# Performance work log

Measured on AMD Instinct MI355X. Metric: run time of the kernel, lower is better.

The kernel has to match this reference:

```python
import jax, jax.numpy as jnp
import numpy as np

N, D_IN, D_OUT = 4096, 1024, 1024

def setup_inputs() -> dict:
    key = jax.random.key(0)
    ks = jax.random.split(key, 7)
    s = 1.0 / np.sqrt(D_IN)
    return {
        "x": jax.random.normal(ks[0], (N, D_IN), dtype=jnp.float32),
        "W1": jax.random.normal(ks[1], (D_OUT, D_IN), dtype=jnp.float32) * s,
        "b1": jax.random.normal(ks[2], (D_OUT,), dtype=jnp.float32) * 0.01,
        "W2": jax.random.normal(ks[3], (D_OUT, D_IN), dtype=jnp.float32) * s,
        "b2": jax.random.normal(ks[4], (D_OUT,), dtype=jnp.float32) * 0.01,
        "W3": jax.random.normal(ks[5], (D_OUT, D_IN), dtype=jnp.float32) * s,
        "b3": jax.random.normal(ks[6], (D_OUT,), dtype=jnp.float32) * 0.01,
        "output_dim": D_OUT,
    }

def reference(x, W1, b1, W2, b2, W3, b3, output_dim):
    # q, k, v: [N, D_OUT]  (torch Linear: x @ W.T + b)
    q = x @ W1.T + b1
    k = x @ W2.T + b2
    v = x @ W3.T + b3
    # NOTE: original computes K @ Q^T (not Q @ K^T) — keep faithful.
    scale = 1.0 / jnp.sqrt(jnp.asarray(output_dim, dtype=x.dtype))
    attn = jax.nn.softmax(jnp.einsum("nd,md->nm", k, q) * scale, axis=-1)  # [N, N]
    # value.unsqueeze(0) * attn.unsqueeze(-1) summed over axis 1 == attn @ v
    return attn @ v  # [N, D_OUT]
```

## Files before the change

kernel.cpp:

```cpp
#include <hip/hip_runtime.h>


typedef short bf16x8 __attribute__((ext_vector_type(8)));
typedef float f32x4  __attribute__((ext_vector_type(4)));

struct FalseT { static constexpr bool value = false; };
struct TrueT  { static constexpr bool value = true;  };

__device__ __forceinline__ short f2bf(float f) {
    unsigned u = __builtin_bit_cast(unsigned, f);
    u += 0x7FFFu + ((u >> 16) & 1u);
    return (short)(u >> 16);
}
__device__ __forceinline__ float bf2f(short s) {
    return __builtin_bit_cast(float, (unsigned)((unsigned short)s) << 16);
}

__device__ __forceinline__ void gld_lds16(const short* g, short* l) {
    __builtin_amdgcn_global_load_lds(
        (const __attribute__((address_space(1))) void*)g,
        (__attribute__((address_space(3))) void*)l, 16, 0, 0);
}

#define WAITV(n) asm volatile("s_waitcnt vmcnt(" #n ")" ::: "memory")
#define LGKM0()  do { asm volatile("s_waitcnt lgkmcnt(0)" ::: "memory"); \
                      __builtin_amdgcn_sched_barrier(0); } while (0)
#define LGKM8()  asm volatile("s_waitcnt lgkmcnt(8)" ::: "memory")
#define BAR()    __builtin_amdgcn_s_barrier()

template<int CMODE>
__global__ __launch_bounds__(512)
void gemm256(const short* __restrict__ A, int lda,
             const short* __restrict__ B, int ldb,
             const float* __restrict__ bias,
             short* __restrict__ Cout, int ldc, float scale,
             int K, size_t zstride)
{
    __shared__ __align__(16) short As[2][2][128 * 64];
    __shared__ __align__(16) short Bs[2][2][128 * 64];

    const int tid  = threadIdx.x;
    const int lane = tid & 63;
    const int wave = tid >> 6;
    const int wr   = wave >> 2;
    const int wc   = wave & 3;
    const int quad = lane >> 4;
    const int l16  = lane & 15;
    const size_t bm0 = (size_t)blockIdx.y * 256;
    const size_t bn0 = (size_t)blockIdx.x * 256;
    const int koff = blockIdx.z * K;

    f32x4 acc[8][4] = {};

    const int srow  = lane >> 3;
    const int sgran = (lane & 7) ^ srow;
    const short* Ag0 = A + (bm0 + wave * 16 + srow) * (size_t)lda + koff + sgran * 8;
    const short* Ag1 = Ag0 + (size_t)128 * lda;
    const short* Bg0 = B + (bn0 + wave * 16 + srow) * (size_t)ldb + koff + sgran * 8;
    const short* Bg1 = Bg0 + (size_t)128 * ldb;

    const int s0   = ((quad ^ (l16 & 7)) << 3);
    const int s1   = (((4 + quad) ^ (l16 & 7)) << 3);
    const int rdA0 = (wr * 64 + l16) * 64;
    const int rdB0 = (wc * 32 + l16) * 64;

    auto stage = [&](short* half, const short* g, int ld, int kt) {
#pragma unroll
        for (int i = 0; i < 2; ++i)
            gld_lds16(g + (size_t)(i * 8) * ld + kt,
                      half + (wave * 16 + i * 8) * 64);
    };

    bf16x8 af[4][2], bfr0[2][2], bfr1[2][2];

    auto ldAf = [&](const short* Ah) {
#pragma unroll
        for (int m4 = 0; m4 < 4; ++m4) {
            af[m4][0] = *(const bf16x8*)(Ah + rdA0 + m4 * 1024 + s0);
            af[m4][1] = *(const bf16x8*)(Ah + rdA0 + m4 * 1024 + s1);
        }
    };
    auto ldBf = [&](bf16x8 (&bx)[2][2], const short* Bh) {
#pragma unroll
        for (int n2 = 0; n2 < 2; ++n2) {
            bx[n2][0] = *(const bf16x8*)(Bh + rdB0 + n2 * 1024 + s0);
            bx[n2][1] = *(const bf16x8*)(Bh + rdB0 + n2 * 1024 + s1);
        }
    };
    auto mm = [&](int mq, int nq, bf16x8 (&bx)[2][2]) {
        __builtin_amdgcn_s_setprio(1);
#pragma unroll
        for (int ks = 0; ks < 2; ++ks)
#pragma unroll
            for (int m4 = 0; m4 < 4; ++m4)
#pragma unroll
                for (int n2 = 0; n2 < 2; ++n2)
                    acc[mq * 4 + m4][nq * 2 + n2] =
                        __builtin_amdgcn_mfma_f32_16x16x32_bf16(
                            af[m4][ks], bx[n2][ks],
                            acc[mq * 4 + m4][nq * 2 + n2], 0, 0, 0);
        __builtin_amdgcn_s_setprio(0);
    };

    stage(&As[0][0][0], Ag0, lda, 0);
    stage(&Bs[0][0][0], Bg0, ldb, 0);
    stage(&Bs[0][1][0], Bg1, ldb, 0);
    stage(&As[0][1][0], Ag1, lda, 0);
    stage(&As[1][0][0], Ag0, lda, 64);
    stage(&Bs[1][0][0], Bg0, ldb, 64);
    stage(&Bs[1][1][0], Bg1, ldb, 64);
    WAITV(6);
    BAR();
    __builtin_amdgcn_sched_barrier(0);

    int kt = 0;
    auto iterbody = [&](auto LASTC) {
        constexpr bool LAST = decltype(LASTC)::value;
        ldAf(&As[0][0][0]);
        ldBf(bfr0, &Bs[0][0][0]);
        stage(&As[1][1][0], Ag1, lda, kt + 64);
        LGKM8();
        BAR();
        LGKM0();
        mm(0, 0, bfr0);
        BAR();
        ldBf(bfr1, &Bs[0][1][0]);
        if constexpr (!LAST) stage(&As[0][0][0], Ag0, lda, kt + 128);
        BAR();
        LGKM0();
        mm(0, 1, bfr1);
        BAR();
        ldAf(&As[0][1][0]);
        if constexpr (!LAST) stage(&Bs[0][0][0], Bg0, ldb, kt + 128);
        BAR();
        LGKM0();
        mm(1, 1, bfr1);
        BAR();
        if constexpr (!LAST) stage(&Bs[0][1][0], Bg1, ldb, kt + 128);
        mm(1, 0, bfr0);
        if constexpr (LAST) { WAITV(0); } else { WAITV(6); }
        BAR();
        ldAf(&As[1][0][0]);
        ldBf(bfr0, &Bs[1][0][0]);
        if constexpr (!LAST) stage(&As[0][1][0], Ag1, lda, kt + 128);
        LGKM8();
        BAR();
        LGKM0();
        mm(0, 0, bfr0);
        BAR();
        ldBf(bfr1, &Bs[1][1][0]);
        if constexpr (!LAST) stage(&As[1][0][0], Ag0, lda, kt + 192);
        BAR();
        LGKM0();
        mm(0, 1, bfr1);
        BAR();
        ldAf(&As[1][1][0]);
        if constexpr (!LAST) stage(&Bs[1][0][0], Bg0, ldb, kt + 192);
        BAR();
        LGKM0();
        mm(1, 1, bfr1);
        BAR();
        if constexpr (!LAST) stage(&Bs[1][1][0], Bg1, ldb, kt + 192);
        mm(1, 0, bfr0);
        if constexpr (!LAST) { WAITV(6); }
        BAR();
    };

    const int nfull = (K >> 7) - 1;
    for (int i = 0; i < nfull; ++i) {
        iterbody(FalseT{});
        kt += 128;
    }
    iterbody(TrueT{});

    short* Cs = Cout + ((CMODE == 3) ? (size_t)blockIdx.z * zstride : 0);
#pragma unroll
    for (int mt = 0; mt < 8; ++mt) {
        const int mq = mt >> 2, m4 = mt & 3;
#pragma unroll
        for (int nt = 0; nt < 4; ++nt) {
            const int nq = nt >> 1, n2 = nt & 1;
            const size_t col = bn0 + nq * 128 + wc * 32 + n2 * 16 + l16;
            const float bc = (CMODE == 0) ? bias[col] : 0.0f;
#pragma unroll
            for (int r = 0; r < 4; ++r) {
                const size_t row = bm0 + mq * 128 + wr * 64 + m4 * 16 + quad * 4 + r;
                float v = acc[mt][nt][r] * scale + bc;
                if (CMODE == 2) v = __expf(v);
                Cs[row * (size_t)ldc + col] = f2bf(v);
            }
        }
    }
}

__global__ __launch_bounds__(256)
void transpose_v(const short* __restrict__ qkv, short* __restrict__ vt)
{
    __shared__ short sh[64][72];
    const int n0 = blockIdx.x * 64, d0 = blockIdx.y * 64;
    const int t = threadIdx.x;
    const int r = t >> 2, c = (t & 3) << 4;

    const short* src = qkv + (size_t)(n0 + r) * 3072 + 2048 + d0 + c;
    *(int4*)(&sh[r][c])     = *(const int4*)(src);
    *(int4*)(&sh[r][c + 8]) = *(const int4*)(src + 8);
    __syncthreads();

    short tmp[16];
#pragma unroll
    for (int j = 0; j < 16; j++) tmp[j] = sh[c + j][r];
    short* dst = vt + (size_t)(d0 + r) * 4096 + n0 + c;
    *(int4*)(dst)     = *(const int4*)(tmp);
    *(int4*)(dst + 8) = *(const int4*)(tmp + 8);
}

__global__ __launch_bounds__(256)
void reduce4div(const short* __restrict__ E, const short* __restrict__ outp,
                float* __restrict__ out)
{
    const int row = blockIdx.x;
    const int t = threadIdx.x;
    const int wave = t >> 6, lane = t & 63;

    const short* e = E + (size_t)row * 4096 + (t << 4);
    short sh[16];
    *(int4*)(sh)     = *(const int4*)(e);
    *(int4*)(sh + 8) = *(const int4*)(e + 8);
    float s = 0.0f;
#pragma unroll
    for (int i = 0; i < 16; i++) s += bf2f(sh[i]);
#pragma unroll
    for (int off = 32; off; off >>= 1) s += __shfl_down(s, off);
    __shared__ float red[4];
    if (lane == 0) red[wave] = s;
    __syncthreads();
    const float inv = 1.0f / (red[0] + red[1] + red[2] + red[3]);

    const size_t base = (size_t)row * 1024 + (t << 2);
    float a[4] = {0.0f, 0.0f, 0.0f, 0.0f};
#pragma unroll
    for (int z = 0; z < 4; z++) {
        short4 p = *(const short4*)(outp + z * (size_t)4096 * 1024 + base);
        a[0] += bf2f(p.x); a[1] += bf2f(p.y);
        a[2] += bf2f(p.z); a[3] += bf2f(p.w);
    }
    float4 o;
    o.x = a[0] * inv; o.y = a[1] * inv; o.z = a[2] * inv; o.w = a[3] * inv;
    *(float4*)(out + base) = o;
}

__global__ __launch_bounds__(256)
void prep(const float* __restrict__ x, const float* __restrict__ W1,
          const float* __restrict__ W2, const float* __restrict__ W3,
          const float* __restrict__ b1, const float* __restrict__ b2,
          const float* __restrict__ b3,
          short* __restrict__ xb, short* __restrict__ Wb,
          float* __restrict__ bcat)
{
    const int i = blockIdx.x * 256 + threadIdx.x;
    const int NX = 1048576;
    const int NW = 262144;
    if (i < NX + 3 * NW) {
        const float* src; short* dst; int j;
        if (i < NX)               { src = x;  dst = xb; j = i; }
        else if (i < NX + NW)     { src = W1; dst = Wb; j = i - NX; }
        else if (i < NX + 2 * NW) { src = W2; dst = Wb + 1048576; j = i - NX - NW; }
        else                      { src = W3; dst = Wb + 2097152; j = i - NX - 2 * NW; }
        const float4 f = ((const float4*)src)[j];
        short4 o;
        o.x = f2bf(f.x); o.y = f2bf(f.y); o.z = f2bf(f.z); o.w = f2bf(f.w);
        *(short4*)(dst + (j << 2)) = o;
    } else {
        const int j = i - (NX + 3 * NW);
        if (j < 3072)
            bcat[j] = (j < 1024) ? b1[j] : (j < 2048 ? b2[j - 1024] : b3[j - 2048]);
    }
}

extern "C" void kernel_launch(void* const* d_in, const int* in_sizes, int n_in,
                              void* d_out, int out_size, void* d_ws, size_t ws_size,
                              hipStream_t stream)
{
    const float* x  = (const float*)d_in[0];
    const float* W1 = (const float*)d_in[1];
    const float* b1 = (const float*)d_in[2];
    const float* W2 = (const float*)d_in[3];
    const float* b2 = (const float*)d_in[4];
    const float* W3 = (const float*)d_in[5];
    const float* b3 = (const float*)d_in[6];
    float* out = (float*)d_out;

    const int N = 4096, D = 1024;

    char* wsb = (char*)d_ws;
    short* vt   = (short*)wsb;
    short* E    = (short*)(wsb + (size_t)8  * 1024 * 1024);
    short* xb   = (short*)(wsb + (size_t)40 * 1024 * 1024);
    short* Wb   = (short*)(wsb + (size_t)48 * 1024 * 1024);
    float* bcat = (float*)(wsb + (size_t)54 * 1024 * 1024);
    short* qkv  = (short*)(wsb + (size_t)54 * 1024 * 1024 + 16384);
    short* outp = (short*)(wsb + (size_t)40 * 1024 * 1024);

    prep<<<(1048576 + 3 * 262144 + 3072 + 255) / 256, 256, 0, stream>>>(
        x, W1, W2, W3, b1, b2, b3, xb, Wb, bcat);

    dim3 gqkv(3 * D / 256, N / 256);
    gemm256<0><<<gqkv, 512, 0, stream>>>(xb, D, Wb, D, bcat,
                                         qkv, 3 * D, 1.0f, D, 0);

    dim3 gt(N / 64, D / 64);
    transpose_v<<<gt, 256, 0, stream>>>(qkv, vt);

    dim3 gs(N / 256, N / 256);
    gemm256<2><<<gs, 512, 0, stream>>>(qkv + D, 3 * D, qkv, 3 * D,
                                       nullptr, E, N, 0.03125f, D, 0);

    dim3 go(D / 256, N / 256, 4);
    gemm256<3><<<go, 512, 0, stream>>>(E, N, vt, N, nullptr,
                                       outp, D, 1.0f, N / 4,
                                       (size_t)N * D);

    reduce4div<<<N, 256, 0, stream>>>(E, outp, out);
}
```

Before: 218.0 us.

## Switch GEMM to 32x32x16 MFMA tiles and drop explicit LDS waits

Replaces the 16x16x32 bf16 MFMA tiling with 32x32x16 instructions, so each wave computes 2x1 32x32 fragments per quadrant with 16-wide accumulators. LDS fragment loads are restructured to match the new operand layout, and the epilogue row/column mapping is rewritten. The explicit lgkmcnt waits and several barriers around fragment loads are removed, leaving the compiler to insert LDS waits, with sched_barriers added after the vmcnt waits. The larger MFMA should cut instruction issue and LDS traffic per FLOP, but it changes the LDS bank-access pattern and risks less overlap or races from the fewer barriers.

```diff
diff --git a/kernel.cpp b/kernel.cpp
--- a/kernel.cpp
+++ b/kernel.cpp
@@ -2,7 +2,7 @@
 
 
 typedef short bf16x8 __attribute__((ext_vector_type(8)));
-typedef float f32x4  __attribute__((ext_vector_type(4)));
+typedef float f32x16 __attribute__((ext_vector_type(16)));
 
 struct FalseT { static constexpr bool value = false; };
 struct TrueT  { static constexpr bool value = true;  };
@@ -23,9 +23,6 @@
 }
 
 #define WAITV(n) asm volatile("s_waitcnt vmcnt(" #n ")" ::: "memory")
-#define LGKM0()  do { asm volatile("s_waitcnt lgkmcnt(0)" ::: "memory"); \
-                      __builtin_amdgcn_sched_barrier(0); } while (0)
-#define LGKM8()  asm volatile("s_waitcnt lgkmcnt(8)" ::: "memory")
 #define BAR()    __builtin_amdgcn_s_barrier()
 
 template<int CMODE>
@@ -44,13 +41,13 @@
     const int wave = tid >> 6;
     const int wr   = wave >> 2;
     const int wc   = wave & 3;
-    const int quad = lane >> 4;
-    const int l16  = lane & 15;
+    const int l32  = lane & 31;
+    const int khalf = lane >> 5;
     const size_t bm0 = (size_t)blockIdx.y * 256;
     const size_t bn0 = (size_t)blockIdx.x * 256;
     const int koff = blockIdx.z * K;
 
-    f32x4 acc[8][4] = {};
+    f32x16 acc[4][2] = {};
 
     const int srow  = lane >> 3;
     const int sgran = (lane & 7) ^ srow;
@@ -59,10 +56,9 @@
     const short* Bg0 = B + (bn0 + wave * 16 + srow) * (size_t)ldb + koff + sgran * 8;
     const short* Bg1 = Bg0 + (size_t)128 * ldb;
 
-    const int s0   = ((quad ^ (l16 & 7)) << 3);
-    const int s1   = (((4 + quad) ^ (l16 & 7)) << 3);
-    const int rdA0 = (wr * 64 + l16) * 64;
-    const int rdB0 = (wc * 32 + l16) * 64;
+    const int sx   = l32 & 7;
+    const int rdA0 = (wr * 64 + l32) * 64;
+    const int rdB0 = (wc * 32 + l32) * 64;
 
     auto stage = [&](short* half, const short* g, int ld, int kt) {
 #pragma unroll
@@ -71,34 +67,30 @@
                       half + (wave * 16 + i * 8) * 64);
     };
 
-    bf16x8 af[4][2], bfr0[2][2], bfr1[2][2];
-
-    auto ldAf = [&](const short* Ah) {
-#pragma unroll
-        for (int m4 = 0; m4 < 4; ++m4) {
-            af[m4][0] = *(const bf16x8*)(Ah + rdA0 + m4 * 1024 + s0);
-            af[m4][1] = *(const bf16x8*)(Ah + rdA0 + m4 * 1024 + s1);
-        }
-    };
-    auto ldBf = [&](bf16x8 (&bx)[2][2], const short* Bh) {
-#pragma unroll
-        for (int n2 = 0; n2 < 2; ++n2) {
-            bx[n2][0] = *(const bf16x8*)(Bh + rdB0 + n2 * 1024 + s0);
-            bx[n2][1] = *(const bf16x8*)(Bh + rdB0 + n2 * 1024 + s1);
-        }
-    };
-    auto mm = [&](int mq, int nq, bf16x8 (&bx)[2][2]) {
+    bf16x8 af[2][4], bfr0[4], bfr1[4];
+
+    auto ldA = [&](const short* Ah) {
+#pragma unroll
+        for (int f = 0; f < 2; ++f)
+#pragma unroll
+            for (int ks = 0; ks < 4; ++ks)
+                af[f][ks] = *(const bf16x8*)(
+                    Ah + rdA0 + f * 2048 + (((ks * 2 + khalf) ^ sx) << 3));
+    };
+    auto ldB = [&](bf16x8 (&bx)[4], const short* Bh) {
+#pragma unroll
+        for (int ks = 0; ks < 4; ++ks)
+            bx[ks] = *(const bf16x8*)(
+                Bh + rdB0 + (((ks * 2 + khalf) ^ sx) << 3));
+    };
+    auto mm = [&](int mq, int nq, bf16x8 (&bx)[4]) {
         __builtin_amdgcn_s_setprio(1);
 #pragma unroll
-        for (int ks = 0; ks < 2; ++ks)
-#pragma unroll
-            for (int m4 = 0; m4 < 4; ++m4)
-#pragma unroll
-                for (int n2 = 0; n2 < 2; ++n2)
-                    acc[mq * 4 + m4][nq * 2 + n2] =
-                        __builtin_amdgcn_mfma_f32_16x16x32_bf16(
-                            af[m4][ks], bx[n2][ks],
-                            acc[mq * 4 + m4][nq * 2 + n2], 0, 0, 0);
+        for (int ks = 0; ks < 4; ++ks)
+#pragma unroll
+            for (int f = 0; f < 2; ++f)
+                acc[mq * 2 + f][nq] = __builtin_amdgcn_mfma_f32_32x32x16_bf16(
+                    af[f][ks], bx[ks], acc[mq * 2 + f][nq], 0, 0, 0);
         __builtin_amdgcn_s_setprio(0);
     };
 
@@ -116,53 +108,43 @@
     int kt = 0;
     auto iterbody = [&](auto LASTC) {
         constexpr bool LAST = decltype(LASTC)::value;
-        ldAf(&As[0][0][0]);
-        ldBf(bfr0, &Bs[0][0][0]);
+        ldB(bfr0, &Bs[0][0][0]);
+        ldA(&As[0][0][0]);
         stage(&As[1][1][0], Ag1, lda, kt + 64);
-        LGKM8();
-        BAR();
-        LGKM0();
         mm(0, 0, bfr0);
         BAR();
-        ldBf(bfr1, &Bs[0][1][0]);
+        ldB(bfr1, &Bs[0][1][0]);
         if constexpr (!LAST) stage(&As[0][0][0], Ag0, lda, kt + 128);
-        BAR();
-        LGKM0();
         mm(0, 1, bfr1);
         BAR();
-        ldAf(&As[0][1][0]);
+        ldA(&As[0][1][0]);
         if constexpr (!LAST) stage(&Bs[0][0][0], Bg0, ldb, kt + 128);
-        BAR();
-        LGKM0();
         mm(1, 1, bfr1);
         BAR();
         if constexpr (!LAST) stage(&Bs[0][1][0], Bg1, ldb, kt + 128);
         mm(1, 0, bfr0);
         if constexpr (LAST) { WAITV(0); } else { WAITV(6); }
-        BAR();
-        ldAf(&As[1][0][0]);
-        ldBf(bfr0, &Bs[1][0][0]);
+        __builtin_amdgcn_sched_barrier(0);
+        BAR();
+        ldB(bfr0, &Bs[1][0][0]);
+        ldA(&As[1][0][0]);
         if constexpr (!LAST) stage(&As[0][1][0], Ag1, lda, kt + 128);
-        LGKM8();
-        BAR();
-        LGKM0();
         mm(0, 0, bfr0);
         BAR();
-        ldBf(bfr1, &Bs[1][1][0]);
+        ldB(bfr1, &Bs[1][1][0]);
         if constexpr (!LAST) stage(&As[1][0][0], Ag0, lda, kt + 192);
-        BAR();
-        LGKM0();
         mm(0, 1, bfr1);
         BAR();
-        ldAf(&As[1][1][0]);
+        ldA(&As[1][1][0]);
         if constexpr (!LAST) stage(&Bs[1][0][0], Bg0, ldb, kt + 192);
-        BAR();
-        LGKM0();
         mm(1, 1, bfr1);
         BAR();
         if constexpr (!LAST) stage(&Bs[1][1][0], Bg1, ldb, kt + 192);
         mm(1, 0, bfr0);
-        if constexpr (!LAST) { WAITV(6); }
+        if constexpr (!LAST) {
+            WAITV(6);
+            __builtin_amdgcn_sched_barrier(0);
+        }
         BAR();
     };
 
@@ -175,19 +157,19 @@
 
     short* Cs = Cout + ((CMODE == 3) ? (size_t)blockIdx.z * zstride : 0);
 #pragma unroll
-    for (int mt = 0; mt < 8; ++mt) {
-        const int mq = mt >> 2, m4 = mt & 3;
-#pragma unroll
-        for (int nt = 0; nt < 4; ++nt) {
-            const int nq = nt >> 1, n2 = nt & 1;
-            const size_t col = bn0 + nq * 128 + wc * 32 + n2 * 16 + l16;
+    for (int mf = 0; mf < 4; ++mf) {
+        const int mq = mf >> 1, f = mf & 1;
+#pragma unroll
+        for (int nq = 0; nq < 2; ++nq) {
+            const size_t col = bn0 + nq * 128 + wc * 32 + l32;
             const float bc = (CMODE == 0) ? bias[col] : 0.0f;
 #pragma unroll
-            for (int r = 0; r < 4; ++r) {
-                const size_t row = bm0 + mq * 128 + wr * 64 + m4 * 16 + quad * 4 + r;
-                float v = acc[mt][nt][r] * scale + bc;
-                if (CMODE == 2) v = __expf(v);
-                Cs[row * (size_t)ldc + col] = f2bf(v);
+            for (int v = 0; v < 16; ++v) {
+                const size_t row = bm0 + mq * 128 + wr * 64 + f * 32 +
+                                   (v & 3) + ((v >> 2) << 3) + khalf * 4;
+                float val = acc[mf][nq][v] * scale + bc;
+                if (CMODE == 2) val = __expf(val);
+                Cs[row * (size_t)ldc + col] = f2bf(val);
             }
         }
     }
```

Measured after the change: 224.1 us. 1.03x slower.
